# Performance work log

Hardware: AMD Instinct MI355X
Metric: run time of the kernel (lower is better)

Reference implementation:

```python
import jax, jax.numpy as jnp
import numpy as np

MARGIN = 1.0

def setup_inputs() -> dict:
    key = jax.random.key(0)
    k1, k2 = jax.random.split(key)
    B, C = 1024, 128
    logits = jax.random.normal(k1, (B, C), dtype=jnp.float32)
    targets = jax.random.bernoulli(k2, 0.05, (B, C)).astype(jnp.float32)
    return {"logits": logits, "targets": targets}

def reference(logits, targets):
    # probs: [B, C]
    probs = jax.nn.sigmoid(logits)
    pos = (targets > 0.5).astype(probs.dtype)  # [B, C]
    neg = (targets < 0.5).astype(probs.dtype)  # [B, C]
    # pairwise diff over batch, per class: [B, B, C]
    diff = probs[:, None, :] - probs[None, :, :]
    # log(1 + exp(-m * diff)) == softplus(-m * diff)
    pair = jax.nn.softplus(-MARGIN * diff)  # [B, B, C]
    # masked sum: only (pos i, neg j) pairs count, per class
    num = jnp.einsum('ijc,ic,jc->c', pair, pos, neg)  # [C]
    n_pos = pos.sum(axis=0)  # [C]
    n_neg = neg.sum(axis=0)  # [C]
    cnt = n_pos * n_neg
    valid = cnt > 0
    per_class_mean = jnp.where(valid, num / jnp.maximum(cnt, 1.0), 0.0)  # [C]
    vcount = valid.sum().astype(probs.dtype)
    loss = jnp.where(vcount > 0, per_class_mean.sum() / jnp.maximum(vcount, 1.0), 0.0)
    return loss
```

## Files before the change

kernel.cpp:

```cpp
#include <hip/hip_runtime.h>


#define NMOM 9

__global__ __launch_bounds__(256) void aucm_moments_kernel(
    const float* __restrict__ logits,
    const float* __restrict__ targets,
    float* __restrict__ ws,
    int B, int C)
{
    const int c   = blockIdx.x;
    const int tid = threadIdx.x;

    float pm[NMOM], nm[NMOM];
#pragma unroll
    for (int k = 0; k < NMOM; ++k) { pm[k] = 0.0f; nm[k] = 0.0f; }

    for (int b = tid; b < B; b += 256) {
        const float l = logits[b * C + c];
        const float t = targets[b * C + c];
        const float p = 1.0f / (1.0f + __expf(-l));
        const bool isPos = (t > 0.5f);
        float pw = 1.0f;
#pragma unroll
        for (int k = 0; k < NMOM; ++k) {
            if (isPos) pm[k] += pw; else nm[k] += pw;
            pw *= p;
        }
    }

    const int lane = tid & 63;
    const int wave = tid >> 6;
    __shared__ float red[2 * NMOM][4];

#pragma unroll
    for (int k = 0; k < NMOM; ++k) {
        float v = pm[k];
#pragma unroll
        for (int off = 32; off > 0; off >>= 1) v += __shfl_down(v, off);
        if (lane == 0) red[k][wave] = v;
        float w = nm[k];
#pragma unroll
        for (int off = 32; off > 0; off >>= 1) w += __shfl_down(w, off);
        if (lane == 0) red[NMOM + k][wave] = w;
    }
    __syncthreads();

    if (tid == 0) {
        float A[NMOM], Bv[NMOM];
#pragma unroll
        for (int k = 0; k < NMOM; ++k) {
            A[k]  = red[k][0] + red[k][1] + red[k][2] + red[k][3];
            Bv[k] = red[NMOM + k][0] + red[NMOM + k][1] + red[NMOM + k][2] + red[NMOM + k][3];
        }
        const float s1 = A[1]*Bv[0] - A[0]*Bv[1];
        const float s2 = A[2]*Bv[0] - 2.0f*A[1]*Bv[1] + A[0]*Bv[2];
        const float s4 = A[4]*Bv[0] - 4.0f*A[3]*Bv[1] + 6.0f*A[2]*Bv[2]
                       - 4.0f*A[1]*Bv[3] + A[0]*Bv[4];
        const float s6 = A[6]*Bv[0] - 6.0f*A[5]*Bv[1] + 15.0f*A[4]*Bv[2]
                       - 20.0f*A[3]*Bv[3] + 15.0f*A[2]*Bv[4] - 6.0f*A[1]*Bv[5]
                       + A[0]*Bv[6];
        const float s8 = A[8]*Bv[0] - 8.0f*A[7]*Bv[1] + 28.0f*A[6]*Bv[2]
                       - 56.0f*A[5]*Bv[3] + 70.0f*A[4]*Bv[4] - 56.0f*A[3]*Bv[5]
                       + 28.0f*A[2]*Bv[6] - 8.0f*A[1]*Bv[7] + A[0]*Bv[8];

        const float cnt = A[0] * Bv[0];
        const float num = 0.69314718056f * cnt
                        - 0.5f            * s1
                        + 0.125f          * s2
                        - 5.20833333e-3f  * s4
                        + 3.47222222e-4f  * s6
                        - 2.63516865e-5f  * s8;

        const bool valid = (cnt > 0.0f);
        ws[c]     = valid ? num / fmaxf(cnt, 1.0f) : 0.0f;
        ws[C + c] = valid ? 1.0f : 0.0f;
    }
}

__global__ __launch_bounds__(128) void aucm_finalize_kernel(
    const float* __restrict__ ws, float* __restrict__ out, int C)
{
    const int tid = threadIdx.x;
    float m = (tid < C) ? ws[tid]     : 0.0f;
    float v = (tid < C) ? ws[C + tid] : 0.0f;
#pragma unroll
    for (int off = 32; off > 0; off >>= 1) {
        m += __shfl_down(m, off);
        v += __shfl_down(v, off);
    }
    __shared__ float sm[2], sv[2];
    const int lane = tid & 63, wave = tid >> 6;
    if (lane == 0) { sm[wave] = m; sv[wave] = v; }
    __syncthreads();
    if (tid == 0) {
        const float ms = sm[0] + sm[1];
        const float vs = sv[0] + sv[1];
        out[0] = (vs > 0.0f) ? ms / fmaxf(vs, 1.0f) : 0.0f;
    }
}

extern "C" void kernel_launch(void* const* d_in, const int* in_sizes, int n_in,
                              void* d_out, int out_size, void* d_ws, size_t ws_size,
                              hipStream_t stream) {
    const float* logits  = (const float*)d_in[0];
    const float* targets = (const float*)d_in[1];
    float* ws  = (float*)d_ws;
    float* out = (float*)d_out;

    const int C = 128;
    const int B = in_sizes[0] / C;

    aucm_moments_kernel<<<C, 256, 0, stream>>>(logits, targets, ws, B, C);
    aucm_finalize_kernel<<<1, 128, 0, stream>>>(ws, out, C);
}
```

Before: 62.49 us.

## Fuse moments and finalize into one cooperative kernel with grid sync

```diff
diff --git a/kernel.cpp b/kernel.cpp
--- a/kernel.cpp
+++ b/kernel.cpp
@@ -1,30 +1,35 @@
 #include <hip/hip_runtime.h>
+#include <hip/hip_cooperative_groups.h>
+
+namespace cg = cooperative_groups;
 
 
 #define NMOM 9
 
-__global__ __launch_bounds__(256) void aucm_moments_kernel(
+__global__ __launch_bounds__(256) void aucm_fused_kernel(
     const float* __restrict__ logits,
     const float* __restrict__ targets,
     float* __restrict__ ws,
+    float* __restrict__ out,
     int B, int C)
 {
     const int c   = blockIdx.x;
     const int tid = threadIdx.x;
 
-    float pm[NMOM], nm[NMOM];
+    float pm[NMOM];
+    float sm[NMOM];
 #pragma unroll
-    for (int k = 0; k < NMOM; ++k) { pm[k] = 0.0f; nm[k] = 0.0f; }
+    for (int k = 0; k < NMOM; ++k) { pm[k] = 0.0f; sm[k] = 0.0f; }
 
     for (int b = tid; b < B; b += 256) {
         const float l = logits[b * C + c];
         const float t = targets[b * C + c];
         const float p = 1.0f / (1.0f + __expf(-l));
-        const bool isPos = (t > 0.5f);
         float pw = 1.0f;
 #pragma unroll
         for (int k = 0; k < NMOM; ++k) {
-            if (isPos) pm[k] += pw; else nm[k] += pw;
+            sm[k] += pw;
+            pm[k] = fmaf(t, pw, pm[k]);
             pw *= p;
         }
     }
@@ -39,7 +44,7 @@
 #pragma unroll
         for (int off = 32; off > 0; off >>= 1) v += __shfl_down(v, off);
         if (lane == 0) red[k][wave] = v;
-        float w = nm[k];
+        float w = sm[k];
 #pragma unroll
         for (int off = 32; off > 0; off >>= 1) w += __shfl_down(w, off);
         if (lane == 0) red[NMOM + k][wave] = w;
@@ -50,8 +55,10 @@
         float A[NMOM], Bv[NMOM];
 #pragma unroll
         for (int k = 0; k < NMOM; ++k) {
-            A[k]  = red[k][0] + red[k][1] + red[k][2] + red[k][3];
-            Bv[k] = red[NMOM + k][0] + red[NMOM + k][1] + red[NMOM + k][2] + red[NMOM + k][3];
+            A[k] = red[k][0] + red[k][1] + red[k][2] + red[k][3];
+            const float s = red[NMOM + k][0] + red[NMOM + k][1]
+                          + red[NMOM + k][2] + red[NMOM + k][3];
+            Bv[k] = s - A[k];
         }
         const float s1 = A[1]*Bv[0] - A[0]*Bv[1];
         const float s2 = A[2]*Bv[0] - 2.0f*A[1]*Bv[1] + A[0]*Bv[2];
@@ -72,31 +79,35 @@
                         + 3.47222222e-4f  * s6
                         - 2.63516865e-5f  * s8;
 
-        const bool valid = (cnt > 0.0f);
-        ws[c]     = valid ? num / fmaxf(cnt, 1.0f) : 0.0f;
-        ws[C + c] = valid ? 1.0f : 0.0f;
+        const bool  valid = (cnt > 0.0f);
+        const float mean  = valid ? num / fmaxf(cnt, 1.0f) : 0.0f;
+        const float vf    = valid ? 1.0f : 0.0f;
+
+        __hip_atomic_store(&ws[c],     mean, __ATOMIC_RELAXED, __HIP_MEMORY_SCOPE_AGENT);
+        __hip_atomic_store(&ws[C + c], vf,   __ATOMIC_RELAXED, __HIP_MEMORY_SCOPE_AGENT);
     }
-}
 
-__global__ __launch_bounds__(128) void aucm_finalize_kernel(
-    const float* __restrict__ ws, float* __restrict__ out, int C)
-{
-    const int tid = threadIdx.x;
-    float m = (tid < C) ? ws[tid]     : 0.0f;
-    float v = (tid < C) ? ws[C + tid] : 0.0f;
+    cg::this_grid().sync();
+
+    if (blockIdx.x == 0) {
+        float m = 0.0f, v = 0.0f;
+        if (tid < C) {
+            m = __hip_atomic_load(&ws[tid],     __ATOMIC_RELAXED, __HIP_MEMORY_SCOPE_AGENT);
+            v = __hip_atomic_load(&ws[C + tid], __ATOMIC_RELAXED, __HIP_MEMORY_SCOPE_AGENT);
+        }
 #pragma unroll
-    for (int off = 32; off > 0; off >>= 1) {
-        m += __shfl_down(m, off);
-        v += __shfl_down(v, off);
-    }
-    __shared__ float sm[2], sv[2];
-    const int lane = tid & 63, wave = tid >> 6;
-    if (lane == 0) { sm[wave] = m; sv[wave] = v; }
-    __syncthreads();
-    if (tid == 0) {
-        const float ms = sm[0] + sm[1];
-        const float vs = sv[0] + sv[1];
-        out[0] = (vs > 0.0f) ? ms / fmaxf(vs, 1.0f) : 0.0f;
+        for (int off = 32; off > 0; off >>= 1) {
+            m += __shfl_down(m, off);
+            v += __shfl_down(v, off);
+        }
+        __shared__ float sm2[4], sv2[4];
+        if (lane == 0) { sm2[wave] = m; sv2[wave] = v; }
+        __syncthreads();
+        if (tid == 0) {
+            const float ms = sm2[0] + sm2[1] + sm2[2] + sm2[3];
+            const float vs = sv2[0] + sv2[1] + sv2[2] + sv2[3];
+            out[0] = (vs > 0.0f) ? ms / fmaxf(vs, 1.0f) : 0.0f;
+        }
     }
 }
 
@@ -108,9 +119,11 @@
     float* ws  = (float*)d_ws;
     float* out = (float*)d_out;
 
-    const int C = 128;
-    const int B = in_sizes[0] / C;
+    int C = 128;
+    int B = in_sizes[0] / C;
 
-    aucm_moments_kernel<<<C, 256, 0, stream>>>(logits, targets, ws, B, C);
-    aucm_finalize_kernel<<<1, 128, 0, stream>>>(ws, out, C);
+    void* args[] = { (void*)&logits, (void*)&targets, (void*)&ws, (void*)&out,
+                     (void*)&B, (void*)&C };
+    hipLaunchCooperativeKernel((void*)aucm_fused_kernel, dim3(C), dim3(256),
+                               args, 0, stream);
 }
```

New measurement: 90.42 us. 44.7% more time.
